# Performance work log

Measured on AMD Instinct MI355X. Metric: run time of the kernel, lower is better.

## Reference

```python
import jax, jax.numpy as jnp
import numpy as np

# Clause structure: 4 unary clauses and 4 binary (joined-space) clauses,
# each with 3 literals; first literal negated ('n' prefix).
U_IDX = np.array([[0, 1, 2], [3, 4, 5], [6, 7, 8], [9, 10, 11]], dtype=np.int32)
U_SIGNS = np.array([[-1.0, 1.0, 1.0]] * 4, dtype=np.float32)
# Joined matrix columns: [u[i1] (0..15), u[i2] (16..31), binary (32..35)]
B_IDX = np.array([[0, 16, 32], [1, 17, 33], [2, 18, 34], [3, 19, 35]], dtype=np.int32)
B_SIGNS = np.array([[-1.0, 1.0, 1.0]] * 4, dtype=np.float32)

N_NODES, N_UNARY = 50000, 16
N_EDGES, N_BINARY = 1600000, 4
INIT_W = 0.5


def setup_inputs() -> dict:
    key = jax.random.key(0)
    k1, k2, k3, k4 = jax.random.split(key, 4)
    unary = jax.random.normal(k1, (N_NODES, N_UNARY), dtype=jnp.float32)
    binary = jax.random.normal(k2, (N_EDGES, N_BINARY), dtype=jnp.float32)
    edge_index = jax.random.randint(k3, (2, N_EDGES), 0, N_NODES, dtype=jnp.int32)
    wu = jnp.full((4,), INIT_W, dtype=jnp.float32)  # learnable unary clause weights
    wb = jnp.full((4,), INIT_W, dtype=jnp.float32)  # learnable binary clause weights
    return {"unary": unary, "binary": binary, "wu": wu, "wb": wb, "edge_index": edge_index}


def _knowledge_enhancer(x, idx, signs, w):
    """x: [R, P]; idx/signs: [C, L]; w: [C]. Returns summed deltas [R, P]."""
    lit = x[:, idx] * signs                                    # [R, C, L] signed literals
    d = (w[:, None] * jax.nn.softmax(lit, axis=-1)) * signs    # [R, C, L] signed deltas
    return jnp.zeros_like(x).at[:, idx].add(d)                 # scatter-sum over clauses


def reference(unary, binary, wu, wb, edge_index):
    i1, i2 = edge_index[0], edge_index[1]
    P = unary.shape[1]
    # Unary knowledge enhancement
    u = unary + _knowledge_enhancer(unary, U_IDX, U_SIGNS, wu)
    # Join: per-edge [u[i1] | u[i2] | binary]
    joined = jnp.concatenate([u[i1], u[i2], binary], axis=1)   # [E, 2P+B]
    d = _knowledge_enhancer(joined, B_IDX, B_SIGNS, wb)        # [E, 2P+B]
    # GroupBy: scatter node blocks back, keep binary block
    n = unary.shape[0]
    delta_up = (jax.ops.segment_sum(d[:, :P], i1, num_segments=n)
                + jax.ops.segment_sum(d[:, P:2 * P], i2, num_segments=n))
    delta_bp = d[:, 2 * P:]
    # activation = identity (default)
    return u + delta_up, binary + delta_bp
```

## Files before the change

kernel.cpp:

```cpp
#include <hip/hip_runtime.h>

#define N_NODES 50000
#define N_UNARY 16
#define N_EDGES 1600000
#define N_BINARY 4

typedef float vfloat4 __attribute__((ext_vector_type(4)));

#define FP_SCALE 127.0f
#define FP_INV   (1.0f / 127.0f)

#define BUCKET_SHIFT 11
#define BUCKET_NODES 2048
#define N_BUCKETS 25
#define N_GROUPS 50
#define SEG_CAP 73728
#define N_CHUNKS 10

#define TAILS_STRIDE 16

#define SCAT_BLOCK 1024
#define SCAT_EPT 4
#define SCAT_EDGES (SCAT_BLOCK * SCAT_EPT)
#define SCAT_RECS (2 * SCAT_EDGES)

#define SEG_BYTES   ((size_t)N_GROUPS * SEG_CAP * 8)
#define TAILS_BYTES ((size_t)4096)
#define ACC_BYTES   ((size_t)N_NODES * 2 * 8)
#define UE_BYTES    ((size_t)N_NODES * 16)
#define WS_NEEDED   (SEG_BYTES + TAILS_BYTES + ACC_BYTES + UE_BYTES)
#define WS_MIN      ((size_t)2 * N_NODES * 8)

__device__ inline void enhance_u4(const float x[6], float wu0, float wu1,
                                  float u[4]) {
    float l0 = -x[0], l1 = x[1], l2 = x[2];
    float m  = fmaxf(l0, fmaxf(l1, l2));
    float e0 = __expf(l0 - m), e1 = __expf(l1 - m), e2 = __expf(l2 - m);
    float inv = 1.0f / (e0 + e1 + e2);
    u[0] = x[0] - wu0 * e0 * inv;
    u[1] = x[1] + wu0 * e1 * inv;
    u[2] = x[2] + wu0 * e2 * inv;
    float l3 = -x[3], l4 = x[4], l5 = x[5];
    float m2 = fmaxf(l3, fmaxf(l4, l5));
    float f0 = __expf(l3 - m2), f1 = __expf(l4 - m2), f2 = __expf(l5 - m2);
    float inv2 = 1.0f / (f0 + f1 + f2);
    u[3] = x[3] - wu1 * f0 * inv2;
}

__device__ inline unsigned long long make_rec(const float s[4], unsigned idg) {
    unsigned v0 = __float2uint_rn(s[0] * FP_SCALE);
    unsigned v1 = __float2uint_rn(s[1] * FP_SCALE);
    unsigned v2 = __float2uint_rn(s[2] * FP_SCALE);
    unsigned v3 = __float2uint_rn(s[3] * FP_SCALE);
    unsigned pl = v0 | (v1 << 7) | (v2 << 14) | (v3 << 21);
    return (unsigned long long)pl | ((unsigned long long)idg << 28);
}

__device__ inline unsigned long long pack4_16(const float s[4]) {
    unsigned long long a = __float2uint_rn(s[0] * FP_SCALE);
    unsigned long long b = __float2uint_rn(s[1] * FP_SCALE);
    unsigned long long c = __float2uint_rn(s[2] * FP_SCALE);
    unsigned long long d = __float2uint_rn(s[3] * FP_SCALE);
    return a | (b << 16) | (c << 32) | (d << 48);
}

__device__ inline void edge_core(const float4* __restrict__ ue,
                                 const float* __restrict__ binary,
                                 const float wc[4], int i1, int i2, int e,
                                 float s0[4], float s1[4],
                                 float* __restrict__ out_b) {
    float4 av = ue[i1];
    float4 bv = ue[i2];
    float a[4] = {av.x, av.y, av.z, av.w};
    float b[4] = {bv.x, bv.y, bv.z, bv.w};
    vfloat4 bn = __builtin_nontemporal_load((const vfloat4*)binary + e);
    float bb[4] = {bn.x, bn.y, bn.z, bn.w};
    float ob[4];
#pragma unroll
    for (int c = 0; c < 4; ++c) {
        float l0 = -a[c], l1 = b[c], l2 = bb[c];
        float m  = fmaxf(l0, fmaxf(l1, l2));
        float e0 = __expf(l0 - m);
        float e1 = __expf(l1 - m);
        float e2 = __expf(l2 - m);
        float inv = 1.0f / (e0 + e1 + e2);
        s0[c] = e0 * inv;
        s1[c] = e1 * inv;
        ob[c] = bb[c] + wc[c] * e2 * inv;
    }
    vfloat4 obv = {ob[0], ob[1], ob[2], ob[3]};
    __builtin_nontemporal_store(obv, (vfloat4*)out_b + e);
}

__global__ void __launch_bounds__(256)
kenn_pre_kernel(const float* __restrict__ unary,
                const float* __restrict__ wu,
                float4* __restrict__ ue,
                unsigned* __restrict__ tails,
                unsigned long long* __restrict__ accN,
                unsigned long long* __restrict__ accP) {
    int n = blockIdx.x * 256 + threadIdx.x;
    if (n < N_GROUPS) tails[n * TAILS_STRIDE] = 0u;
    if (n >= N_NODES) return;
    accN[n] = 0ull;
    accP[n] = 0ull;
    const float4* up = (const float4*)(unary + (size_t)n * N_UNARY);
    float4 x0 = up[0], x1 = up[1];
    float x[6] = {x0.x, x0.y, x0.z, x0.w, x1.x, x1.y};
    float u[4];
    enhance_u4(x, wu[0], wu[1], u);
    ue[n] = make_float4(u[0], u[1], u[2], u[3]);
}

__global__ void __launch_bounds__(SCAT_BLOCK)
kenn_edge_scatter_kernel(const float4* __restrict__ ue,
                         const float* __restrict__ binary,
                         const float* __restrict__ wb,
                         const int* __restrict__ edge_index,
                         unsigned long long* __restrict__ segs,
                         unsigned* __restrict__ tails,
                         float* __restrict__ out_b) {
    __shared__ unsigned l_cnt[N_GROUPS];
    __shared__ unsigned l_pref[N_GROUPS + 1];
    __shared__ unsigned l_gbase[N_GROUPS];
    __shared__ unsigned long long staged[SCAT_RECS];

    int tid = threadIdx.x;
    if (tid < N_GROUPS) l_cnt[tid] = 0;
    __syncthreads();

    int base = blockIdx.x * SCAT_EDGES;
    float wc[4] = {wb[0], wb[1], wb[2], wb[3]};

    bool valid[SCAT_EPT];
    unsigned posg1[SCAT_EPT], posg2[SCAT_EPT];
    unsigned long long rec1[SCAT_EPT], rec2[SCAT_EPT];

#pragma unroll
    for (int k = 0; k < SCAT_EPT; ++k) {
        int e = base + k * SCAT_BLOCK + tid;
        valid[k] = (e < N_EDGES);
        if (!valid[k]) continue;
        int i1 = __builtin_nontemporal_load(edge_index + e);
        int i2 = __builtin_nontemporal_load(edge_index + N_EDGES + e);
        float s0[4], s1[4];
        edge_core(ue, binary, wc, i1, i2, e, s0, s1, out_b);
        unsigned g1 = (unsigned)(i1 >> BUCKET_SHIFT);
        unsigned g2 = N_BUCKETS + (unsigned)(i2 >> BUCKET_SHIFT);
        rec1[k] = make_rec(s0, (unsigned)(i1 & (BUCKET_NODES - 1)) | (g1 << 11));
        rec2[k] = make_rec(s1, (unsigned)(i2 & (BUCKET_NODES - 1)) | (g2 << 11));
        unsigned p1 = atomicAdd(&l_cnt[g1], 1u);
        unsigned p2 = atomicAdd(&l_cnt[g2], 1u);
        posg1[k] = (p1 << 6) | g1;
        posg2[k] = (p2 << 6) | g2;
    }
    __syncthreads();

    if (tid < 64) {
        unsigned c = (tid < N_GROUPS) ? l_cnt[tid] : 0u;
        unsigned s = c;
#pragma unroll
        for (int off = 1; off < 64; off <<= 1) {
            unsigned o = __shfl_up(s, off, 64);
            if (tid >= off) s += o;
        }
        if (tid < N_GROUPS) l_pref[tid] = s - c;
        if (tid == N_GROUPS - 1) l_pref[N_GROUPS] = s;
    } else if (tid >= 64 && tid < 64 + N_GROUPS) {
        int g = tid - 64;
        unsigned c = l_cnt[g];
        l_gbase[g] = c ? atomicAdd(tails + g * TAILS_STRIDE, c) : 0u;
    }
    __syncthreads();

#pragma unroll
    for (int k = 0; k < SCAT_EPT; ++k) {
        if (!valid[k]) continue;
        unsigned g1 = posg1[k] & 63u, p1 = l_pref[g1] + (posg1[k] >> 6);
        unsigned g2 = posg2[k] & 63u, p2 = l_pref[g2] + (posg2[k] >> 6);
        staged[p1] = rec1[k];
        staged[p2] = rec2[k];
    }
    __syncthreads();

    unsigned total = l_pref[N_GROUPS];
    for (unsigned i = tid; i < total; i += SCAT_BLOCK) {
        unsigned long long rec = staged[i];
        unsigned g = (unsigned)(rec >> 39) & 63u;
        unsigned p = l_gbase[g] + (i - l_pref[g]);
        if (p < SEG_CAP)
            __builtin_nontemporal_store(rec, segs + (size_t)g * SEG_CAP + p);
    }
}

__global__ void __launch_bounds__(512)
kenn_reduce_kernel(const unsigned long long* __restrict__ segs,
                   const unsigned* __restrict__ tails,
                   unsigned long long* __restrict__ accN,
                   unsigned long long* __restrict__ accP) {
    __shared__ unsigned long long lacc[BUCKET_NODES];
    int chunk = blockIdx.x;
    int g     = blockIdx.y;
    int tid   = threadIdx.x;

    for (int i = tid; i < BUCKET_NODES; i += blockDim.x) lacc[i] = 0ull;
    __syncthreads();

    unsigned cnt = tails[g * TAILS_STRIDE];
    if (cnt > SEG_CAP) cnt = SEG_CAP;
    unsigned csz   = (cnt + N_CHUNKS - 1) / N_CHUNKS;
    unsigned start = chunk * csz;
    unsigned end   = start + csz;
    if (end > cnt) end = cnt;

    const unsigned long long* seg = segs + (size_t)g * SEG_CAP;
    for (unsigned i = start + tid; i < end; i += blockDim.x) {
        unsigned long long r = seg[i];
        unsigned id = (unsigned)(r >> 28) & (BUCKET_NODES - 1);
        unsigned pl = (unsigned)r & 0x0FFFFFFFu;
        unsigned long long exp =
            (unsigned long long)(pl & 127u) |
            ((unsigned long long)(pl & (127u << 7))  << 9)  |
            ((unsigned long long)(pl & (127u << 14)) << 18) |
            ((unsigned long long)(pl & (127u << 21)) << 27);
        atomicAdd(&lacc[id], exp);
    }
    __syncthreads();

    int bucket = (g < N_BUCKETS) ? g : (g - N_BUCKETS);
    unsigned long long* acc =
        ((g < N_BUCKETS) ? accN : accP) + (size_t)bucket * BUCKET_NODES;
    for (int i = tid; i < BUCKET_NODES; i += blockDim.x) {
        unsigned long long v = lacc[i];
        if (v) atomicAdd(acc + i, v);
    }
}

__global__ void __launch_bounds__(256)
kenn_node_final_kernel(const float* __restrict__ unary,
                       const float* __restrict__ wu,
                       const float* __restrict__ wb,
                       const unsigned long long* __restrict__ accN,
                       const unsigned long long* __restrict__ accP,
                       float* __restrict__ out_u) {
    int node = blockIdx.x * 256 + threadIdx.x;
    if (node >= N_NODES) return;

    const float4* up = (const float4*)(unary + (size_t)node * N_UNARY);
    float4 x0 = up[0], x1 = up[1], x2 = up[2], x3 = up[3];
    float x[16] = {x0.x, x0.y, x0.z, x0.w,
                   x1.x, x1.y, x1.z, x1.w,
                   x2.x, x2.y, x2.z, x2.w,
                   x3.x, x3.y, x3.z, x3.w};
    float wuc[4] = {wu[0], wu[1], wu[2], wu[3]};

    float y[16];
#pragma unroll
    for (int i = 0; i < 16; ++i) y[i] = x[i];

#pragma unroll
    for (int c = 0; c < 4; ++c) {
        float l0 = -x[3 * c + 0];
        float l1 =  x[3 * c + 1];
        float l2 =  x[3 * c + 2];
        float m  = fmaxf(l0, fmaxf(l1, l2));
        float e0 = __expf(l0 - m);
        float e1 = __expf(l1 - m);
        float e2 = __expf(l2 - m);
        float inv = 1.0f / (e0 + e1 + e2);
        y[3 * c + 0] -= wuc[c] * e0 * inv;
        y[3 * c + 1] += wuc[c] * e1 * inv;
        y[3 * c + 2] += wuc[c] * e2 * inv;
    }

    unsigned long long pn = accN[node];
    unsigned long long pp = accP[node];

    float wbc[4] = {wb[0], wb[1], wb[2], wb[3]};
    y[0] += wbc[0] * ((float)(int)((pp      ) & 0xffff) - (float)(int)((pn      ) & 0xffff)) * FP_INV;
    y[1] += wbc[1] * ((float)(int)((pp >> 16) & 0xffff) - (float)(int)((pn >> 16) & 0xffff)) * FP_INV;
    y[2] += wbc[2] * ((float)(int)((pp >> 32) & 0xffff) - (float)(int)((pn >> 32) & 0xffff)) * FP_INV;
    y[3] += wbc[3] * ((float)(int)((pp >> 48) & 0xffff) - (float)(int)((pn >> 48) & 0xffff)) * FP_INV;

    float4* op = (float4*)(out_u + (size_t)node * N_UNARY);
    op[0] = make_float4(y[0],  y[1],  y[2],  y[3]);
    op[1] = make_float4(y[4],  y[5],  y[6],  y[7]);
    op[2] = make_float4(y[8],  y[9],  y[10], y[11]);
    op[3] = make_float4(y[12], y[13], y[14], y[15]);
}

__global__ void kenn_edge_atomic_noue_kernel(const float* __restrict__ unary,
                                             const float* __restrict__ binary,
                                             const float* __restrict__ wu,
                                             const float* __restrict__ wb,
                                             const int* __restrict__ edge_index,
                                             unsigned long long* __restrict__ acc,
                                             float* __restrict__ out_b) {
    int e = blockIdx.x * blockDim.x + threadIdx.x;
    if (e >= N_EDGES) return;
    int i1 = __builtin_nontemporal_load(edge_index + e);
    int i2 = __builtin_nontemporal_load(edge_index + N_EDGES + e);
    float wu0 = wu[0], wu1 = wu[1];
    float wc[4] = {wb[0], wb[1], wb[2], wb[3]};

    const float4* u1p = (const float4*)(unary + (size_t)i1 * N_UNARY);
    const float4* u2p = (const float4*)(unary + (size_t)i2 * N_UNARY);
    float4 x1a = u1p[0], x1b = u1p[1];
    float4 x2a = u2p[0], x2b = u2p[1];
    float xa[6] = {x1a.x, x1a.y, x1a.z, x1a.w, x1b.x, x1b.y};
    float xb[6] = {x2a.x, x2a.y, x2a.z, x2a.w, x2b.x, x2b.y};
    float a[4], b[4];
    enhance_u4(xa, wu0, wu1, a);
    enhance_u4(xb, wu0, wu1, b);

    vfloat4 bn = __builtin_nontemporal_load((const vfloat4*)binary + e);
    float bb[4] = {bn.x, bn.y, bn.z, bn.w};
    float s0[4], s1[4], ob[4];
#pragma unroll
    for (int c = 0; c < 4; ++c) {
        float l0 = -a[c], l1 = b[c], l2 = bb[c];
        float m  = fmaxf(l0, fmaxf(l1, l2));
        float e0 = __expf(l0 - m);
        float e1 = __expf(l1 - m);
        float e2 = __expf(l2 - m);
        float inv = 1.0f / (e0 + e1 + e2);
        s0[c] = e0 * inv;
        s1[c] = e1 * inv;
        ob[c] = bb[c] + wc[c] * e2 * inv;
    }
    vfloat4 obv = {ob[0], ob[1], ob[2], ob[3]};
    __builtin_nontemporal_store(obv, (vfloat4*)out_b + e);

    atomicAdd(acc + i1, pack4_16(s0));
    atomicAdd(acc + (size_t)N_NODES + i2, pack4_16(s1));
}

__global__ void __launch_bounds__(256)
kenn_node_final_flat_kernel(const float* __restrict__ unary,
                            const float* __restrict__ wu,
                            const float* __restrict__ wb,
                            const unsigned long long* __restrict__ acc,
                            float* __restrict__ out_u) {
    int node = blockIdx.x * 256 + threadIdx.x;
    if (node >= N_NODES) return;

    const float4* up = (const float4*)(unary + (size_t)node * N_UNARY);
    float4 x0 = up[0], x1 = up[1], x2 = up[2], x3 = up[3];
    float x[16] = {x0.x, x0.y, x0.z, x0.w,
                   x1.x, x1.y, x1.z, x1.w,
                   x2.x, x2.y, x2.z, x2.w,
                   x3.x, x3.y, x3.z, x3.w};
    float wuc[4] = {wu[0], wu[1], wu[2], wu[3]};

    float y[16];
#pragma unroll
    for (int i = 0; i < 16; ++i) y[i] = x[i];

#pragma unroll
    for (int c = 0; c < 4; ++c) {
        float l0 = -x[3 * c + 0];
        float l1 =  x[3 * c + 1];
        float l2 =  x[3 * c + 2];
        float m  = fmaxf(l0, fmaxf(l1, l2));
        float e0 = __expf(l0 - m);
        float e1 = __expf(l1 - m);
        float e2 = __expf(l2 - m);
        float inv = 1.0f / (e0 + e1 + e2);
        y[3 * c + 0] -= wuc[c] * e0 * inv;
        y[3 * c + 1] += wuc[c] * e1 * inv;
        y[3 * c + 2] += wuc[c] * e2 * inv;
    }

    unsigned long long pn = acc[node];
    unsigned long long pp = acc[(size_t)N_NODES + node];

    float wbc[4] = {wb[0], wb[1], wb[2], wb[3]};
    y[0] += wbc[0] * ((float)(int)((pp      ) & 0xffff) - (float)(int)((pn      ) & 0xffff)) * FP_INV;
    y[1] += wbc[1] * ((float)(int)((pp >> 16) & 0xffff) - (float)(int)((pn >> 16) & 0xffff)) * FP_INV;
    y[2] += wbc[2] * ((float)(int)((pp >> 32) & 0xffff) - (float)(int)((pn >> 32) & 0xffff)) * FP_INV;
    y[3] += wbc[3] * ((float)(int)((pp >> 48) & 0xffff) - (float)(int)((pn >> 48) & 0xffff)) * FP_INV;

    float4* op = (float4*)(out_u + (size_t)node * N_UNARY);
    op[0] = make_float4(y[0],  y[1],  y[2],  y[3]);
    op[1] = make_float4(y[4],  y[5],  y[6],  y[7]);
    op[2] = make_float4(y[8],  y[9],  y[10], y[11]);
    op[3] = make_float4(y[12], y[13], y[14], y[15]);
}

extern "C" void kernel_launch(void* const* d_in, const int* in_sizes, int n_in,
                              void* d_out, int out_size, void* d_ws, size_t ws_size,
                              hipStream_t stream) {
    const float* unary      = (const float*)d_in[0];
    const float* binary     = (const float*)d_in[1];
    const float* wu         = (const float*)d_in[2];
    const float* wb         = (const float*)d_in[3];
    const int*   edge_index = (const int*)d_in[4];

    float* out_u = (float*)d_out;
    float* out_b = (float*)d_out + (size_t)N_NODES * N_UNARY;

    if (ws_size >= WS_NEEDED) {
        unsigned long long* segs = (unsigned long long*)d_ws;
        unsigned* tails = (unsigned*)((char*)d_ws + SEG_BYTES);
        unsigned long long* accN =
            (unsigned long long*)((char*)d_ws + SEG_BYTES + TAILS_BYTES);
        unsigned long long* accP = accN + N_NODES;
        float4* ue =
            (float4*)((char*)d_ws + SEG_BYTES + TAILS_BYTES + ACC_BYTES);

        {
            dim3 grid((N_NODES + 255) / 256);
            kenn_pre_kernel<<<grid, dim3(256), 0, stream>>>(
                unary, wu, ue, tails, accN, accP);
        }
        {
            dim3 grid((N_EDGES + SCAT_EDGES - 1) / SCAT_EDGES);
            kenn_edge_scatter_kernel<<<grid, dim3(SCAT_BLOCK), 0, stream>>>(
                ue, binary, wb, edge_index, segs, tails, out_b);
        }
        {
            dim3 grid(N_CHUNKS, N_GROUPS);
            kenn_reduce_kernel<<<grid, dim3(512), 0, stream>>>(
                segs, tails, accN, accP);
        }
        {
            dim3 grid((N_NODES + 255) / 256);
            kenn_node_final_kernel<<<grid, dim3(256), 0, stream>>>(
                unary, wu, wb, accN, accP, out_u);
        }
    } else {
        unsigned long long* acc = (unsigned long long*)d_ws;
        (void)hipMemsetAsync(acc, 0, WS_MIN, stream);
        {
            dim3 block(256);
            dim3 grid((N_EDGES + 255) / 256);
            kenn_edge_atomic_noue_kernel<<<grid, block, 0, stream>>>(
                unary, binary, wu, wb, edge_index, acc, out_b);
        }
        {
            dim3 grid((N_NODES + 255) / 256);
            kenn_node_final_flat_kernel<<<grid, dim3(256), 0, stream>>>(
                unary, wu, wb, acc, out_u);
        }
    }
}
```

Before: 145.5 us.

## Batch edge index and gather loads ahead of compute, halve scatter block size

The edge scatter kernel now issues all edge index loads for its four edges per thread first, then all gathers of enhanced unary rows and binary rows, and only then runs the softmax and record-packing work. This puts many independent memory requests in flight per thread so gather latency is hidden. The block size drops from 1024 to 512 with a launch-bounds occupancy hint of 4, which changes the per-block shared staging size and adds register pressure from the held loads. Out-of-range edges are clamped to a valid index so the loads can be issued unconditionally.

```diff
diff --git a/kernel.cpp b/kernel.cpp
--- a/kernel.cpp
+++ b/kernel.cpp
@@ -19,7 +19,7 @@
 
 #define TAILS_STRIDE 16
 
-#define SCAT_BLOCK 1024
+#define SCAT_BLOCK 512
 #define SCAT_EPT 4
 #define SCAT_EDGES (SCAT_BLOCK * SCAT_EPT)
 #define SCAT_RECS (2 * SCAT_EDGES)
@@ -62,34 +62,6 @@
     unsigned long long c = __float2uint_rn(s[2] * FP_SCALE);
     unsigned long long d = __float2uint_rn(s[3] * FP_SCALE);
     return a | (b << 16) | (c << 32) | (d << 48);
-}
-
-__device__ inline void edge_core(const float4* __restrict__ ue,
-                                 const float* __restrict__ binary,
-                                 const float wc[4], int i1, int i2, int e,
-                                 float s0[4], float s1[4],
-                                 float* __restrict__ out_b) {
-    float4 av = ue[i1];
-    float4 bv = ue[i2];
-    float a[4] = {av.x, av.y, av.z, av.w};
-    float b[4] = {bv.x, bv.y, bv.z, bv.w};
-    vfloat4 bn = __builtin_nontemporal_load((const vfloat4*)binary + e);
-    float bb[4] = {bn.x, bn.y, bn.z, bn.w};
-    float ob[4];
-#pragma unroll
-    for (int c = 0; c < 4; ++c) {
-        float l0 = -a[c], l1 = b[c], l2 = bb[c];
-        float m  = fmaxf(l0, fmaxf(l1, l2));
-        float e0 = __expf(l0 - m);
-        float e1 = __expf(l1 - m);
-        float e2 = __expf(l2 - m);
-        float inv = 1.0f / (e0 + e1 + e2);
-        s0[c] = e0 * inv;
-        s1[c] = e1 * inv;
-        ob[c] = bb[c] + wc[c] * e2 * inv;
-    }
-    vfloat4 obv = {ob[0], ob[1], ob[2], ob[3]};
-    __builtin_nontemporal_store(obv, (vfloat4*)out_b + e);
 }
 
 __global__ void __launch_bounds__(256)
@@ -112,7 +84,7 @@
     ue[n] = make_float4(u[0], u[1], u[2], u[3]);
 }
 
-__global__ void __launch_bounds__(SCAT_BLOCK)
+__global__ void __launch_bounds__(SCAT_BLOCK, 4)
 kenn_edge_scatter_kernel(const float4* __restrict__ ue,
                          const float* __restrict__ binary,
                          const float* __restrict__ wb,
@@ -133,22 +105,57 @@
     float wc[4] = {wb[0], wb[1], wb[2], wb[3]};
 
     bool valid[SCAT_EPT];
-    unsigned posg1[SCAT_EPT], posg2[SCAT_EPT];
-    unsigned long long rec1[SCAT_EPT], rec2[SCAT_EPT];
+    int idx1[SCAT_EPT], idx2[SCAT_EPT];
 
 #pragma unroll
     for (int k = 0; k < SCAT_EPT; ++k) {
         int e = base + k * SCAT_BLOCK + tid;
         valid[k] = (e < N_EDGES);
+        int ec = valid[k] ? e : (N_EDGES - 1);
+        idx1[k] = __builtin_nontemporal_load(edge_index + ec);
+        idx2[k] = __builtin_nontemporal_load(edge_index + N_EDGES + ec);
+    }
+
+    float4 av[SCAT_EPT], bv[SCAT_EPT];
+    vfloat4 bn[SCAT_EPT];
+#pragma unroll
+    for (int k = 0; k < SCAT_EPT; ++k) {
+        av[k] = ue[idx1[k]];
+        bv[k] = ue[idx2[k]];
+        int e = base + k * SCAT_BLOCK + tid;
+        int ec = valid[k] ? e : (N_EDGES - 1);
+        bn[k] = __builtin_nontemporal_load((const vfloat4*)binary + ec);
+    }
+
+    unsigned posg1[SCAT_EPT], posg2[SCAT_EPT];
+    unsigned long long rec1[SCAT_EPT], rec2[SCAT_EPT];
+#pragma unroll
+    for (int k = 0; k < SCAT_EPT; ++k) {
         if (!valid[k]) continue;
-        int i1 = __builtin_nontemporal_load(edge_index + e);
-        int i2 = __builtin_nontemporal_load(edge_index + N_EDGES + e);
-        float s0[4], s1[4];
-        edge_core(ue, binary, wc, i1, i2, e, s0, s1, out_b);
-        unsigned g1 = (unsigned)(i1 >> BUCKET_SHIFT);
-        unsigned g2 = N_BUCKETS + (unsigned)(i2 >> BUCKET_SHIFT);
-        rec1[k] = make_rec(s0, (unsigned)(i1 & (BUCKET_NODES - 1)) | (g1 << 11));
-        rec2[k] = make_rec(s1, (unsigned)(i2 & (BUCKET_NODES - 1)) | (g2 << 11));
+        int e = base + k * SCAT_BLOCK + tid;
+        float a4[4] = {av[k].x, av[k].y, av[k].z, av[k].w};
+        float b4[4] = {bv[k].x, bv[k].y, bv[k].z, bv[k].w};
+        float bb[4] = {bn[k].x, bn[k].y, bn[k].z, bn[k].w};
+        float s0[4], s1[4], ob[4];
+#pragma unroll
+        for (int c = 0; c < 4; ++c) {
+            float l0 = -a4[c], l1 = b4[c], l2 = bb[c];
+            float m  = fmaxf(l0, fmaxf(l1, l2));
+            float e0 = __expf(l0 - m);
+            float e1 = __expf(l1 - m);
+            float e2 = __expf(l2 - m);
+            float inv = 1.0f / (e0 + e1 + e2);
+            s0[c] = e0 * inv;
+            s1[c] = e1 * inv;
+            ob[c] = bb[c] + wc[c] * e2 * inv;
+        }
+        vfloat4 obv = {ob[0], ob[1], ob[2], ob[3]};
+        __builtin_nontemporal_store(obv, (vfloat4*)out_b + e);
+
+        unsigned g1 = (unsigned)(idx1[k] >> BUCKET_SHIFT);
+        unsigned g2 = N_BUCKETS + (unsigned)(idx2[k] >> BUCKET_SHIFT);
+        rec1[k] = make_rec(s0, (unsigned)(idx1[k] & (BUCKET_NODES - 1)) | (g1 << 11));
+        rec2[k] = make_rec(s1, (unsigned)(idx2[k] & (BUCKET_NODES - 1)) | (g2 << 11));
         unsigned p1 = atomicAdd(&l_cnt[g1], 1u);
         unsigned p2 = atomicAdd(&l_cnt[g2], 1u);
         posg1[k] = (p1 << 6) | g1;
```

New measurement: 144.5 us. No clear change (-0.6%).
